# Optimization experiments

Measured on AMD Instinct MI355X. Metric: run time of the kernel, lower is better.

The kernel has to match this reference:

```python
import jax, jax.numpy as jnp
import numpy as np


def _build_levels():
    # build_power_value(B=4): w_bit=5 -> B=4 additive-powers-of-two codebook
    value_a = [0.0] + [2.0 ** (-2 * i - 1) for i in range(3)]
    value_b = [0.0] + [2.0 ** (-2 * i - 2) for i in range(3)]
    sums = sorted({a + b for a in value_a for b in value_b})
    levels = np.asarray(sums, dtype=np.float32)
    return jnp.asarray(levels / levels.max())  # 16 levels in [0, 1]


def setup_inputs() -> dict:
    key = jax.random.key(0)
    weight = jax.random.normal(key, (4096, 4096), dtype=jnp.float32) * 0.05
    wgt_alpha = jnp.asarray(2.0, dtype=jnp.float32)
    return {"weight": weight, "wgt_alpha": wgt_alpha}


def reference(weight, wgt_alpha):
    levels = _build_levels()
    # stats are computed on weight.data in torch (detached)
    mean = jax.lax.stop_gradient(jnp.mean(weight))
    std = jax.lax.stop_gradient(jnp.std(weight, ddof=1))  # torch .std() is unbiased
    wn = (weight - mean) / std
    x = wn / wgt_alpha
    xc = jnp.clip(x, -1.0, 1.0)
    sign = jnp.sign(xc)
    # nearest-level search over the 16-entry codebook (first-min tie-break like torch)
    idx = jnp.argmin(jnp.abs(jnp.abs(xc)[..., None] - levels), axis=-1)
    q = levels[idx] * sign
    return q * wgt_alpha
```

## Files before the change

kernel.cpp:

```cpp
#include <hip/hip_runtime.h>
#include <math.h>

#define THREADS 256

typedef float f2v __attribute__((ext_vector_type(2)));
typedef float f4v __attribute__((ext_vector_type(4)));

static constexpr float kLvl[16] = {
    0.0f      / 0.75f, 0.015625f / 0.75f, 0.03125f / 0.75f, 0.046875f / 0.75f,
    0.0625f   / 0.75f, 0.09375f  / 0.75f, 0.125f   / 0.75f, 0.140625f / 0.75f,
    0.1875f   / 0.75f, 0.25f     / 0.75f, 0.28125f / 0.75f, 0.375f    / 0.75f,
    0.5f      / 0.75f, 0.515625f / 0.75f, 0.5625f  / 0.75f, 0.75f     / 0.75f,
};
static constexpr double kMid[15] = {
    ((double)kLvl[0]  + (double)kLvl[1])  * 0.5, ((double)kLvl[1]  + (double)kLvl[2])  * 0.5,
    ((double)kLvl[2]  + (double)kLvl[3])  * 0.5, ((double)kLvl[3]  + (double)kLvl[4])  * 0.5,
    ((double)kLvl[4]  + (double)kLvl[5])  * 0.5, ((double)kLvl[5]  + (double)kLvl[6])  * 0.5,
    ((double)kLvl[6]  + (double)kLvl[7])  * 0.5, ((double)kLvl[7]  + (double)kLvl[8])  * 0.5,
    ((double)kLvl[8]  + (double)kLvl[9])  * 0.5, ((double)kLvl[9]  + (double)kLvl[10]) * 0.5,
    ((double)kLvl[10] + (double)kLvl[11]) * 0.5, ((double)kLvl[11] + (double)kLvl[12]) * 0.5,
    ((double)kLvl[12] + (double)kLvl[13]) * 0.5, ((double)kLvl[13] + (double)kLvl[14]) * 0.5,
    ((double)kLvl[14] + (double)kLvl[15]) * 0.5,
};

__device__ __forceinline__ float tree64(float v) {
    #pragma unroll
    for (int m = 1; m <= 32; m <<= 1)
        v += __shfl_xor(v, m, 64);
    return v;
}

__device__ __forceinline__ float sgpr_bcast(float x) {
    return __uint_as_float(__builtin_amdgcn_readfirstlane(__float_as_uint(x)));
}

#define QSEL(V, RES) do {                                   \
    float _u  = (V) - mean;                                 \
    float _au = fabsf(_u);                                  \
    float _o  = c0;                                         \
    _o = (_au < t0)  ? _o : c1;                             \
    _o = (_au < t1)  ? _o : c2;                             \
    _o = (_au < t2)  ? _o : c3;                             \
    _o = (_au < t3)  ? _o : c4;                             \
    _o = (_au < t4)  ? _o : c5;                             \
    _o = (_au < t5)  ? _o : c6;                             \
    _o = (_au < t6)  ? _o : c7;                             \
    _o = (_au < t7)  ? _o : c8;                             \
    _o = (_au < t8)  ? _o : c9;                             \
    _o = (_au < t9)  ? _o : c10;                            \
    _o = (_au < t10) ? _o : c11;                            \
    _o = (_au < t11) ? _o : c12;                            \
    _o = (_au < t12) ? _o : c13;                            \
    _o = (_au < t13) ? _o : c14;                            \
    _o = (_au < t14) ? _o : c15;                            \
    RES = copysignf(_o, _u);                                \
} while (0)

#define QTAB(V, RES) do {                                            \
    float _u  = (V) - mean;                                          \
    float _au = __uint_as_float(__float_as_uint(_u) & 0x7fffffffu);  \
    unsigned _i = (unsigned)(_au * invH);                            \
    _i = _i > 127u ? 127u : _i;                                      \
    f4v _e = *(const f4v*)&tbl[_i][0];                               \
    float _o = (_au < _e.x) ? _e.y : _e.z;                           \
    RES = copysignf(_o, _u);                                         \
} while (0)

#define HOIST_TC()                                                        \
    const float t0  = sgpr_bcast(sT[0]),  t1  = sgpr_bcast(sT[1]);        \
    const float t2  = sgpr_bcast(sT[2]),  t3  = sgpr_bcast(sT[3]);        \
    const float t4  = sgpr_bcast(sT[4]),  t5  = sgpr_bcast(sT[5]);        \
    const float t6  = sgpr_bcast(sT[6]),  t7  = sgpr_bcast(sT[7]);        \
    const float t8  = sgpr_bcast(sT[8]),  t9  = sgpr_bcast(sT[9]);        \
    const float t10 = sgpr_bcast(sT[10]), t11 = sgpr_bcast(sT[11]);       \
    const float t12 = sgpr_bcast(sT[12]), t13 = sgpr_bcast(sT[13]);       \
    const float t14 = sgpr_bcast(sT[14]);                                 \
    const float c0  = sgpr_bcast(sC[0]),  c1  = sgpr_bcast(sC[1]);        \
    const float c2  = sgpr_bcast(sC[2]),  c3  = sgpr_bcast(sC[3]);        \
    const float c4  = sgpr_bcast(sC[4]),  c5  = sgpr_bcast(sC[5]);        \
    const float c6  = sgpr_bcast(sC[6]),  c7  = sgpr_bcast(sC[7]);        \
    const float c8  = sgpr_bcast(sC[8]),  c9  = sgpr_bcast(sC[9]);        \
    const float c10 = sgpr_bcast(sC[10]), c11 = sgpr_bcast(sC[11]);       \
    const float c12 = sgpr_bcast(sC[12]), c13 = sgpr_bcast(sC[13]);       \
    const float c14 = sgpr_bcast(sC[14]), c15 = sgpr_bcast(sC[15]);

#define THRESH_SETUP(TID)                                                 \
    if ((TID) < 15) {                                                     \
        const double mid = kMid[(TID)];                                   \
        unsigned lo = 0u, hi = 0x7F800000u;                               \
        while (lo < hi) {                                                 \
            unsigned m = (lo + hi) >> 1;                                  \
            float uu = __uint_as_float(m);                                \
            float y  = uu / sd;                                           \
            float x  = y / al;                                            \
            float xc = fminf(x, 1.0f);                                    \
            if ((double)xc > mid) hi = m; else lo = m + 1;                \
        }                                                                 \
        sT[(TID)] = __uint_as_float(lo);                                  \
    } else if ((TID) < 31) {                                              \
        sC[(TID) - 15] = kLvl[(TID) - 15] * al;                           \
    } else if ((TID) == 31) {                                             \
        sC[0] = 0.0f;                                                     \
    }

template<int PASS, int REV>
__global__ __launch_bounds__(THREADS) void leaf_pass(const float* __restrict__ w,
                                                     const float* __restrict__ bprev,
                                                     float* __restrict__ bout,
                                                     long long n, int nb) {
    #pragma clang fp contract(off)
    __shared__ float ws4[4];
    __shared__ float smean;
    float mean = 0.0f;
    if (PASS == 1) {
        int i0 = threadIdx.x * 8;
        float v = 0.0f;
        if (i0 + 7 < nb) {
            const float* p = bprev + i0;
            v = ((p[0] + p[1]) + (p[2] + p[3])) + ((p[4] + p[5]) + (p[6] + p[7]));
        }
        v = tree64(v);
        if ((threadIdx.x & 63) == 0) ws4[threadIdx.x >> 6] = v;
        __syncthreads();
        if (threadIdx.x == 0)
            smean = ((ws4[0] + ws4[1]) + (ws4[2] + ws4[3])) / (float)n;
        __syncthreads();
        mean = smean;
    }
    int region = blockIdx.x;
    if (REV && (nb & 7) == 0) {
        int j = blockIdx.x >> 3;
        region = (blockIdx.x & 7) + 8 * ((nb >> 3) - 1 - j);
    }
    const long long base = (long long)region * 8192
                         + (long long)(threadIdx.x >> 2) * 128
                         + (long long)(threadIdx.x & 3) * 2;
    const f2v* p = (const f2v*)(w + base);
    float s0, s1;
    {
        f2v a = p[0];
        if (PASS == 1) { float x = a.x - mean, y = a.y - mean; s0 = x * x; s1 = y * y; }
        else           { s0 = a.x; s1 = a.y; }
    }
    #pragma unroll
    for (int t = 1; t < 16; ++t) {
        f2v a = p[4 * t];
        if (PASS == 1) { float x = a.x - mean, y = a.y - mean; s0 += x * x; s1 += y * y; }
        else           { s0 += a.x; s1 += a.y; }
    }
    float s = s0 + s1;
    s = tree64(s);
    if ((threadIdx.x & 63) == 0) ws4[threadIdx.x >> 6] = s;
    __syncthreads();
    if (threadIdx.x == 0)
        bout[region] = (ws4[0] + ws4[1]) + (ws4[2] + ws4[3]);
}

__global__ __launch_bounds__(THREADS) void quantize_b(const f4v* __restrict__ w4,
                                                      f4v* __restrict__ o4,
                                                      const float* __restrict__ bout0,
                                                      const float* __restrict__ bout1,
                                                      const float* __restrict__ alpha_ptr,
                                                      long long n, int nb) {
    #pragma clang fp contract(off)
    __shared__ float wsA[4], wsB[4];
    __shared__ float sP[2];
    __shared__ float sT[15];
    __shared__ float sC[16];
    __shared__ float sInvH;
    __shared__ float tbl[128][4];
    {
        int i0 = threadIdx.x * 8;
        float v = 0.0f, u = 0.0f;
        if (i0 + 7 < nb) {
            const float* p0 = bout0 + i0;
            const float* p1 = bout1 + i0;
            v = ((p0[0] + p0[1]) + (p0[2] + p0[3])) + ((p0[4] + p0[5]) + (p0[6] + p0[7]));
            u = ((p1[0] + p1[1]) + (p1[2] + p1[3])) + ((p1[4] + p1[5]) + (p1[6] + p1[7]));
        }
        v = tree64(v);
        u = tree64(u);
        if ((threadIdx.x & 63) == 0) { wsA[threadIdx.x >> 6] = v; wsB[threadIdx.x >> 6] = u; }
        __syncthreads();
        if (threadIdx.x == 0) {
            sP[0] = ((wsA[0] + wsA[1]) + (wsA[2] + wsA[3])) / (float)n;
            sP[1] = sqrtf(((wsB[0] + wsB[1]) + (wsB[2] + wsB[3])) / (float)(n - 1));
        }
        __syncthreads();
    }
    {
        const float sd = sP[1];
        const float al = alpha_ptr[0];
        THRESH_SETUP(threadIdx.x)
    }
    __syncthreads();
    if (threadIdx.x == 0) sInvH = 120.0f / sT[14];
    __syncthreads();
    const float invH = sgpr_bcast(sInvH);
    if (threadIdx.x < 128) {
        const int b = threadIdx.x;
        int base = 0;
        float Tq = __builtin_inff();
        #pragma unroll
        for (int k = 0; k < 15; ++k) {
            float Tk = sT[k];
            unsigned bk = (unsigned)(Tk * invH);
            bk = bk > 127u ? 127u : bk;
            if (bk < (unsigned)b) base++;
            if (bk == (unsigned)b) Tq = Tk;
        }
        int hi = base + 1 <= 15 ? base + 1 : 15;
        tbl[b][0] = Tq;
        tbl[b][1] = sC[base];
        tbl[b][2] = sC[hi];
        tbl[b][3] = 0.0f;
    }
    __syncthreads();

    const float mean = sgpr_bcast(sP[0]);

    const long long base = (long long)blockIdx.x * 2048 + threadIdx.x;
    f4v a0 = w4[base];
    f4v a1 = w4[base + 256];
    f4v a2 = w4[base + 512];
    f4v a3 = w4[base + 768];
    f4v a4 = w4[base + 1024];
    f4v a5 = w4[base + 1280];
    f4v a6 = w4[base + 1536];
    f4v a7 = w4[base + 1792];
    f4v r;
    QTAB(a0.x, r.x); QTAB(a0.y, r.y); QTAB(a0.z, r.z); QTAB(a0.w, r.w);
    __builtin_nontemporal_store(r, &o4[base]);
    QTAB(a1.x, r.x); QTAB(a1.y, r.y); QTAB(a1.z, r.z); QTAB(a1.w, r.w);
    __builtin_nontemporal_store(r, &o4[base + 256]);
    QTAB(a2.x, r.x); QTAB(a2.y, r.y); QTAB(a2.z, r.z); QTAB(a2.w, r.w);
    __builtin_nontemporal_store(r, &o4[base + 512]);
    QTAB(a3.x, r.x); QTAB(a3.y, r.y); QTAB(a3.z, r.z); QTAB(a3.w, r.w);
    __builtin_nontemporal_store(r, &o4[base + 768]);
    QTAB(a4.x, r.x); QTAB(a4.y, r.y); QTAB(a4.z, r.z); QTAB(a4.w, r.w);
    __builtin_nontemporal_store(r, &o4[base + 1024]);
    QTAB(a5.x, r.x); QTAB(a5.y, r.y); QTAB(a5.z, r.z); QTAB(a5.w, r.w);
    __builtin_nontemporal_store(r, &o4[base + 1280]);
    QTAB(a6.x, r.x); QTAB(a6.y, r.y); QTAB(a6.z, r.z); QTAB(a6.w, r.w);
    __builtin_nontemporal_store(r, &o4[base + 1536]);
    QTAB(a7.x, r.x); QTAB(a7.y, r.y); QTAB(a7.z, r.z); QTAB(a7.w, r.w);
    __builtin_nontemporal_store(r, &o4[base + 1792]);
}

__global__ __launch_bounds__(THREADS) void quantize_g(const f4v* __restrict__ w4,
                                                      f4v* __restrict__ o4,
                                                      const float* __restrict__ bout0,
                                                      const float* __restrict__ bout1,
                                                      const float* __restrict__ alpha_ptr,
                                                      long long n, int nb) {
    #pragma clang fp contract(off)
    __shared__ float wsA[4], wsB[4];
    __shared__ float sP[2];
    __shared__ float sT[15];
    __shared__ float sC[16];
    {
        int i0 = threadIdx.x * 8;
        float v = 0.0f, u = 0.0f;
        if (i0 + 7 < nb) {
            const float* p0 = bout0 + i0;
            const float* p1 = bout1 + i0;
            v = ((p0[0] + p0[1]) + (p0[2] + p0[3])) + ((p0[4] + p0[5]) + (p0[6] + p0[7]));
            u = ((p1[0] + p1[1]) + (p1[2] + p1[3])) + ((p1[4] + p1[5]) + (p1[6] + p1[7]));
        }
        v = tree64(v);
        u = tree64(u);
        if ((threadIdx.x & 63) == 0) { wsA[threadIdx.x >> 6] = v; wsB[threadIdx.x >> 6] = u; }
        __syncthreads();
        if (threadIdx.x == 0) {
            sP[0] = ((wsA[0] + wsA[1]) + (wsA[2] + wsA[3])) / (float)n;
            sP[1] = sqrtf(((wsB[0] + wsB[1]) + (wsB[2] + wsB[3])) / (float)(n - 1));
        }
        __syncthreads();
    }
    {
        const float sd = sP[1];
        const float al = alpha_ptr[0];
        THRESH_SETUP(threadIdx.x)
    }
    __syncthreads();

    const float mean = sgpr_bcast(sP[0]);
    HOIST_TC()

    long long n4     = n >> 2;
    long long tid    = (long long)blockIdx.x * THREADS + threadIdx.x;
    long long stride = (long long)gridDim.x * THREADS;
    long long i = tid;
    for (; i + stride < n4; i += 2 * stride) {
        f4v a = w4[i];
        f4v b = w4[i + stride];
        f4v ra, rb;
        QSEL(a.x, ra.x); QSEL(a.y, ra.y); QSEL(a.z, ra.z); QSEL(a.w, ra.w);
        QSEL(b.x, rb.x); QSEL(b.y, rb.y); QSEL(b.z, rb.z); QSEL(b.w, rb.w);
        __builtin_nontemporal_store(ra, &o4[i]);
        __builtin_nontemporal_store(rb, &o4[i + stride]);
    }
    for (; i < n4; i += stride) {
        f4v a = w4[i];
        f4v ra;
        QSEL(a.x, ra.x); QSEL(a.y, ra.y); QSEL(a.z, ra.z); QSEL(a.w, ra.w);
        __builtin_nontemporal_store(ra, &o4[i]);
    }
}

extern "C" void kernel_launch(void* const* d_in, const int* in_sizes, int n_in,
                              void* d_out, int out_size, void* d_ws, size_t ws_size,
                              hipStream_t stream) {
    const float* w     = (const float*)d_in[0];
    const float* alpha = (const float*)d_in[1];
    float* out = (float*)d_out;
    long long n = (long long)in_sizes[0];

    int nblk = (int)(n >> 13);
    float* bout0 = (float*)d_ws;
    float* bout1 = bout0 + nblk;

    leaf_pass<0, 0><<<nblk, THREADS, 0, stream>>>(w, nullptr, bout0, n, nblk);
    leaf_pass<1, 1><<<nblk, THREADS, 0, stream>>>(w, bout0, bout1, n, nblk);
    if (n == (1LL << 24)) {
        quantize_b<<<nblk, THREADS, 0, stream>>>((const f4v*)w, (f4v*)out,
                                                 bout0, bout1, alpha, n, nblk);
    } else {
        quantize_g<<<2048, THREADS, 0, stream>>>((const f4v*)w, (f4v*)out,
                                                 bout0, bout1, alpha, n, nblk);
    }
}
```

Before: 46.24 us.

## Fold global reductions and threshold setup into last-block of leaf kernels

Each leaf pass now atomically counts finished blocks, and the last block performs the global tree reduction. That block writes the mean, or for the second pass the std, the thresholds and the scaled codebook, into a small params buffer. The quantize kernel then just loads 32 precomputed params instead of every block re-reducing the 2048 partials and running the 15-way bisection threshold search. This removes redundant per-block prologue work in quantize and pass 1, at the cost of a memset launch, atomics, and a serial tail in the last block.

```diff
diff --git a/kernel.cpp b/kernel.cpp
--- a/kernel.cpp
+++ b/kernel.cpp
@@ -103,107 +103,132 @@
         sC[0] = 0.0f;                                                     \
     }
 
-template<int PASS, int REV>
-__global__ __launch_bounds__(THREADS) void leaf_pass(const float* __restrict__ w,
-                                                     const float* __restrict__ bprev,
-                                                     float* __restrict__ bout,
-                                                     long long n, int nb) {
-    #pragma clang fp contract(off)
-    __shared__ float ws4[4];
-    __shared__ float smean;
-    float mean = 0.0f;
-    if (PASS == 1) {
-        int i0 = threadIdx.x * 8;
-        float v = 0.0f;
-        if (i0 + 7 < nb) {
-            const float* p = bprev + i0;
-            v = ((p[0] + p[1]) + (p[2] + p[3])) + ((p[4] + p[5]) + (p[6] + p[7]));
-        }
-        v = tree64(v);
-        if ((threadIdx.x & 63) == 0) ws4[threadIdx.x >> 6] = v;
-        __syncthreads();
-        if (threadIdx.x == 0)
-            smean = ((ws4[0] + ws4[1]) + (ws4[2] + ws4[3])) / (float)n;
-        __syncthreads();
-        mean = smean;
-    }
-    int region = blockIdx.x;
-    if (REV && (nb & 7) == 0) {
-        int j = blockIdx.x >> 3;
-        region = (blockIdx.x & 7) + 8 * ((nb >> 3) - 1 - j);
-    }
-    const long long base = (long long)region * 8192
+#define GLOBAL_TREE(PART, OUT) do {                                              \
+    int _i0 = threadIdx.x * 8;                                                   \
+    float _v = 0.0f;                                                             \
+    if (_i0 + 7 < nb) {                                                          \
+        float _p0 = __hip_atomic_load(&(PART)[_i0+0], __ATOMIC_RELAXED, __HIP_MEMORY_SCOPE_AGENT); \
+        float _p1 = __hip_atomic_load(&(PART)[_i0+1], __ATOMIC_RELAXED, __HIP_MEMORY_SCOPE_AGENT); \
+        float _p2 = __hip_atomic_load(&(PART)[_i0+2], __ATOMIC_RELAXED, __HIP_MEMORY_SCOPE_AGENT); \
+        float _p3 = __hip_atomic_load(&(PART)[_i0+3], __ATOMIC_RELAXED, __HIP_MEMORY_SCOPE_AGENT); \
+        float _p4 = __hip_atomic_load(&(PART)[_i0+4], __ATOMIC_RELAXED, __HIP_MEMORY_SCOPE_AGENT); \
+        float _p5 = __hip_atomic_load(&(PART)[_i0+5], __ATOMIC_RELAXED, __HIP_MEMORY_SCOPE_AGENT); \
+        float _p6 = __hip_atomic_load(&(PART)[_i0+6], __ATOMIC_RELAXED, __HIP_MEMORY_SCOPE_AGENT); \
+        float _p7 = __hip_atomic_load(&(PART)[_i0+7], __ATOMIC_RELAXED, __HIP_MEMORY_SCOPE_AGENT); \
+        _v = ((_p0 + _p1) + (_p2 + _p3)) + ((_p4 + _p5) + (_p6 + _p7));          \
+    }                                                                            \
+    _v = tree64(_v);                                                             \
+    if ((threadIdx.x & 63) == 0) ws4[threadIdx.x >> 6] = _v;                     \
+    __syncthreads();                                                             \
+    OUT = (ws4[0] + ws4[1]) + (ws4[2] + ws4[3]);                                 \
+} while (0)
+
+template<int SQ>
+__device__ __forceinline__ float leaf_body(const float* __restrict__ w,
+                                           long long region, float mean) {
+    #pragma clang fp contract(off)
+    const long long base = region * 8192
                          + (long long)(threadIdx.x >> 2) * 128
                          + (long long)(threadIdx.x & 3) * 2;
     const f2v* p = (const f2v*)(w + base);
     float s0, s1;
     {
         f2v a = p[0];
-        if (PASS == 1) { float x = a.x - mean, y = a.y - mean; s0 = x * x; s1 = y * y; }
-        else           { s0 = a.x; s1 = a.y; }
+        if (SQ) { float x = a.x - mean, y = a.y - mean; s0 = x * x; s1 = y * y; }
+        else    { s0 = a.x; s1 = a.y; }
     }
     #pragma unroll
     for (int t = 1; t < 16; ++t) {
         f2v a = p[4 * t];
-        if (PASS == 1) { float x = a.x - mean, y = a.y - mean; s0 += x * x; s1 += y * y; }
-        else           { s0 += a.x; s1 += a.y; }
-    }
-    float s = s0 + s1;
-    s = tree64(s);
+        if (SQ) { float x = a.x - mean, y = a.y - mean; s0 += x * x; s1 += y * y; }
+        else    { s0 += a.x; s1 += a.y; }
+    }
+    return tree64(s0 + s1);
+}
+
+__global__ __launch_bounds__(THREADS) void leaf0F(const float* __restrict__ w,
+                                                  float* __restrict__ bout,
+                                                  float* __restrict__ params,
+                                                  int* __restrict__ cnt,
+                                                  long long n, int nb) {
+    #pragma clang fp contract(off)
+    __shared__ float ws4[4];
+    __shared__ int sLast;
+    float s = leaf_body<0>(w, blockIdx.x, 0.0f);
     if ((threadIdx.x & 63) == 0) ws4[threadIdx.x >> 6] = s;
     __syncthreads();
-    if (threadIdx.x == 0)
-        bout[region] = (ws4[0] + ws4[1]) + (ws4[2] + ws4[3]);
-}
-
-__global__ __launch_bounds__(THREADS) void quantize_b(const f4v* __restrict__ w4,
-                                                      f4v* __restrict__ o4,
-                                                      const float* __restrict__ bout0,
-                                                      const float* __restrict__ bout1,
-                                                      const float* __restrict__ alpha_ptr,
-                                                      long long n, int nb) {
-    #pragma clang fp contract(off)
-    __shared__ float wsA[4], wsB[4];
-    __shared__ float sP[2];
-    __shared__ float sT[15];
-    __shared__ float sC[16];
-    __shared__ float sInvH;
-    __shared__ float tbl[128][4];
-    {
-        int i0 = threadIdx.x * 8;
-        float v = 0.0f, u = 0.0f;
-        if (i0 + 7 < nb) {
-            const float* p0 = bout0 + i0;
-            const float* p1 = bout1 + i0;
-            v = ((p0[0] + p0[1]) + (p0[2] + p0[3])) + ((p0[4] + p0[5]) + (p0[6] + p0[7]));
-            u = ((p1[0] + p1[1]) + (p1[2] + p1[3])) + ((p1[4] + p1[5]) + (p1[6] + p1[7]));
-        }
-        v = tree64(v);
-        u = tree64(u);
-        if ((threadIdx.x & 63) == 0) { wsA[threadIdx.x >> 6] = v; wsB[threadIdx.x >> 6] = u; }
-        __syncthreads();
-        if (threadIdx.x == 0) {
-            sP[0] = ((wsA[0] + wsA[1]) + (wsA[2] + wsA[3])) / (float)n;
-            sP[1] = sqrtf(((wsB[0] + wsB[1]) + (wsB[2] + wsB[3])) / (float)(n - 1));
-        }
-        __syncthreads();
-    }
-    {
-        const float sd = sP[1];
+    if (threadIdx.x == 0) {
+        float p = (ws4[0] + ws4[1]) + (ws4[2] + ws4[3]);
+        __hip_atomic_store(&bout[blockIdx.x], p, __ATOMIC_RELAXED, __HIP_MEMORY_SCOPE_AGENT);
+        int prev = __hip_atomic_fetch_add(&cnt[0], 1, __ATOMIC_ACQ_REL, __HIP_MEMORY_SCOPE_AGENT);
+        sLast = (prev == nb - 1);
+    }
+    __syncthreads();
+    if (sLast) {
+        float total;
+        GLOBAL_TREE(bout, total);
+        if (threadIdx.x == 0) params[0] = total / (float)n;
+    }
+}
+
+__global__ __launch_bounds__(THREADS) void leaf1F(const float* __restrict__ w,
+                                                  float* __restrict__ bout,
+                                                  float* __restrict__ params,
+                                                  int* __restrict__ cnt,
+                                                  const float* __restrict__ alpha_ptr,
+                                                  long long n, int nb) {
+    #pragma clang fp contract(off)
+    __shared__ float ws4[4];
+    __shared__ int sLast;
+    __shared__ float sSd;
+    __shared__ float sT[15], sC[16];
+    const float mean = params[0];
+    int region = blockIdx.x;
+    if ((nb & 7) == 0) {
+        int j = blockIdx.x >> 3;
+        region = (blockIdx.x & 7) + 8 * ((nb >> 3) - 1 - j);
+    }
+    float s = leaf_body<1>(w, region, mean);
+    if ((threadIdx.x & 63) == 0) ws4[threadIdx.x >> 6] = s;
+    __syncthreads();
+    if (threadIdx.x == 0) {
+        float p = (ws4[0] + ws4[1]) + (ws4[2] + ws4[3]);
+        __hip_atomic_store(&bout[region], p, __ATOMIC_RELAXED, __HIP_MEMORY_SCOPE_AGENT);
+        int prev = __hip_atomic_fetch_add(&cnt[0], 1, __ATOMIC_ACQ_REL, __HIP_MEMORY_SCOPE_AGENT);
+        sLast = (prev == nb - 1);
+    }
+    __syncthreads();
+    if (sLast) {
+        float total;
+        GLOBAL_TREE(bout, total);
+        if (threadIdx.x == 0)
+            sSd = sqrtf(total / (float)(n - 1));
+        __syncthreads();
+        const float sd = sSd;
         const float al = alpha_ptr[0];
         THRESH_SETUP(threadIdx.x)
-    }
-    __syncthreads();
-    if (threadIdx.x == 0) sInvH = 120.0f / sT[14];
-    __syncthreads();
-    const float invH = sgpr_bcast(sInvH);
+        __syncthreads();
+        if (threadIdx.x < 15)       params[1 + threadIdx.x]  = sT[threadIdx.x];
+        else if (threadIdx.x < 32)  params[threadIdx.x]      = sC[threadIdx.x - 16];
+    }
+}
+
+__global__ __launch_bounds__(THREADS) void quantize_bp(const f4v* __restrict__ w4,
+                                                       f4v* __restrict__ o4,
+                                                       const float* __restrict__ params) {
+    #pragma clang fp contract(off)
+    __shared__ float sp[32];
+    __shared__ float tbl[128][4];
+    if (threadIdx.x < 32) sp[threadIdx.x] = params[threadIdx.x];
+    __syncthreads();
+    const float invH = sgpr_bcast(120.0f / sp[15]);
     if (threadIdx.x < 128) {
         const int b = threadIdx.x;
         int base = 0;
         float Tq = __builtin_inff();
         #pragma unroll
         for (int k = 0; k < 15; ++k) {
-            float Tk = sT[k];
+            float Tk = sp[1 + k];
             unsigned bk = (unsigned)(Tk * invH);
             bk = bk > 127u ? 127u : bk;
             if (bk < (unsigned)b) base++;
@@ -211,13 +236,12 @@
         }
         int hi = base + 1 <= 15 ? base + 1 : 15;
         tbl[b][0] = Tq;
-        tbl[b][1] = sC[base];
-        tbl[b][2] = sC[hi];
+        tbl[b][1] = sp[16 + base];
+        tbl[b][2] = sp[16 + hi];
         tbl[b][3] = 0.0f;
     }
     __syncthreads();
-
-    const float mean = sgpr_bcast(sP[0]);
+    const float mean = sgpr_bcast(sp[0]);
 
     const long long base = (long long)blockIdx.x * 2048 + threadIdx.x;
     f4v a0 = w4[base];
@@ -247,6 +271,38 @@
     __builtin_nontemporal_store(r, &o4[base + 1792]);
 }
 
+template<int PASS>
+__global__ __launch_bounds__(THREADS) void leaf_pass(const float* __restrict__ w,
+                                                     const float* __restrict__ bprev,
+                                                     float* __restrict__ bout,
+                                                     long long n, int nb) {
+    #pragma clang fp contract(off)
+    __shared__ float ws4[4];
+    __shared__ float smean;
+    float mean = 0.0f;
+    if (PASS == 1) {
+        int i0 = threadIdx.x * 8;
+        float v = 0.0f;
+        if (i0 + 7 < nb) {
+            const float* p = bprev + i0;
+            v = ((p[0] + p[1]) + (p[2] + p[3])) + ((p[4] + p[5]) + (p[6] + p[7]));
+        }
+        v = tree64(v);
+        if ((threadIdx.x & 63) == 0) ws4[threadIdx.x >> 6] = v;
+        __syncthreads();
+        if (threadIdx.x == 0)
+            smean = ((ws4[0] + ws4[1]) + (ws4[2] + ws4[3])) / (float)n;
+        __syncthreads();
+        mean = smean;
+        __syncthreads();
+    }
+    float s = leaf_body<PASS>(w, blockIdx.x, mean);
+    if ((threadIdx.x & 63) == 0) ws4[threadIdx.x >> 6] = s;
+    __syncthreads();
+    if (threadIdx.x == 0)
+        bout[blockIdx.x] = (ws4[0] + ws4[1]) + (ws4[2] + ws4[3]);
+}
+
 __global__ __launch_bounds__(THREADS) void quantize_g(const f4v* __restrict__ w4,
                                                       f4v* __restrict__ o4,
                                                       const float* __restrict__ bout0,
@@ -317,15 +373,21 @@
     long long n = (long long)in_sizes[0];
 
     int nblk = (int)(n >> 13);
-    float* bout0 = (float*)d_ws;
-    float* bout1 = bout0 + nblk;
-
-    leaf_pass<0, 0><<<nblk, THREADS, 0, stream>>>(w, nullptr, bout0, n, nblk);
-    leaf_pass<1, 1><<<nblk, THREADS, 0, stream>>>(w, bout0, bout1, n, nblk);
-    if (n == (1LL << 24)) {
-        quantize_b<<<nblk, THREADS, 0, stream>>>((const f4v*)w, (f4v*)out,
-                                                 bout0, bout1, alpha, n, nblk);
+    size_t need = 2 * sizeof(int) + (size_t)(2 * nblk + 32) * sizeof(float);
+    if (n == (1LL << 24) && ws_size >= need) {
+        int*   cnt    = (int*)d_ws;
+        float* bout0  = (float*)d_ws + 2;
+        float* bout1  = bout0 + nblk;
+        float* params = bout1 + nblk;
+        hipMemsetAsync(cnt, 0, 2 * sizeof(int), stream);
+        leaf0F<<<nblk, THREADS, 0, stream>>>(w, bout0, params, cnt, n, nblk);
+        leaf1F<<<nblk, THREADS, 0, stream>>>(w, bout1, params, cnt + 1, alpha, n, nblk);
+        quantize_bp<<<nblk, THREADS, 0, stream>>>((const f4v*)w, (f4v*)out, params);
     } else {
+        float* bout0 = (float*)d_ws;
+        float* bout1 = bout0 + nblk;
+        leaf_pass<0><<<nblk, THREADS, 0, stream>>>(w, nullptr, bout0, n, nblk);
+        leaf_pass<1><<<nblk, THREADS, 0, stream>>>(w, bout0, bout1, n, nblk);
         quantize_g<<<2048, THREADS, 0, stream>>>((const f4v*)w, (f4v*)out,
                                                  bout0, bout1, alpha, n, nblk);
     }
```

Result: slower. 168.5 us (+264.3%).
